# Kernel optimization log

Measured on AMD Instinct MI355X. Metric: run time of the kernel, lower is better.

The kernel has to match this reference:

```python
import jax, jax.numpy as jnp
import numpy as np

B, T, I, H, O = 64, 512, 256, 1024, 512
STEPS = 100


def _lstm_cell(x, h, c, Wih, Whh, b):
    # torch gate order: i, f, g, o ; Wih:[4H,in], Whh:[4H,H]
    g = x @ Wih.T + h @ Whh.T + b
    i, f, gg, o = jnp.split(g, 4, axis=-1)
    c = jax.nn.sigmoid(f) * c + jax.nn.sigmoid(i) * jnp.tanh(gg)
    h = jax.nn.sigmoid(o) * jnp.tanh(c)
    return h, c


def setup_inputs() -> dict:
    key = jax.random.key(0)
    ks = jax.random.split(key, 11)
    s = 1.0 / np.sqrt(H)  # torch nn.LSTM init scale
    f32 = jnp.float32
    return {
        "inputs": jax.random.normal(ks[0], (B, T, I), f32),
        "enc_Wih": jax.random.normal(ks[1], (4 * H, I), f32) * s,
        "enc_Whh": jax.random.normal(ks[2], (4 * H, H), f32) * s,
        "enc_bih": jax.random.normal(ks[3], (4 * H,), f32) * s,
        "enc_bhh": jax.random.normal(ks[4], (4 * H,), f32) * s,
        "dec_Wih": jax.random.normal(ks[5], (4 * H, O), f32) * s,
        "dec_Whh": jax.random.normal(ks[6], (4 * H, H), f32) * s,
        "dec_bih": jax.random.normal(ks[7], (4 * H,), f32) * s,
        "dec_bhh": jax.random.normal(ks[8], (4 * H,), f32) * s,
        "fc_W": jax.random.normal(ks[9], (O, H), f32) * s,
        "fc_b": jax.random.normal(ks[10], (O,), f32) * s,
    }


def reference(inputs, enc_Wih, enc_Whh, enc_bih, enc_bhh,
              dec_Wih, dec_Whh, dec_bih, dec_bhh, fc_W, fc_b):
    b_enc = enc_bih + enc_bhh
    b_dec = dec_bih + dec_bhh
    Bz = inputs.shape[0]
    h0 = jnp.zeros((Bz, H), inputs.dtype)
    c0 = jnp.zeros((Bz, H), inputs.dtype)

    # ---- encoder LSTM over time (batch_first input -> scan over T) ----
    def enc_step(carry, x_t):
        h, c = carry
        h, c = _lstm_cell(x_t, h, c, enc_Wih, enc_Whh, b_enc)
        return (h, c), None

    (h, c), _ = jax.lax.scan(enc_step, (h0, c0), inputs.transpose(1, 0, 2))

    def dec_step(carry, _):
        inp, h, c = carry
        h, c = _lstm_cell(inp, h, c, dec_Wih, dec_Whh, b_dec)
        logits = h @ fc_W.T + fc_b                 # [B, O]
        tok = jnp.argmax(logits, axis=-1)          # [B]
        # next decoder input: predicted token index broadcast to feature dim
        nxt = jnp.broadcast_to(tok[:, None].astype(inputs.dtype), (Bz, O))
        return (nxt, h, c), tok

    init_inp = jnp.zeros((Bz, O), inputs.dtype)
    _, toks = jax.lax.scan(dec_step, (init_inp, h, c), None, length=STEPS)
    # toks: [STEPS, B] -> [B, STEPS, 1] to match torch cat of (B,1,1) tokens
    return toks.T[:, :, None].astype(jnp.int64)
```

## Files before the change

### kernel.cpp

```cpp
#include <hip/hip_runtime.h>
#include <cstdint>
#include <cmath>

#define BB 64
#define TT 512
#define NI 256
#define HH 1024
#define NO 512
#define NSTEPS 100
#define KT 64
#define NBLK 256
#define NTHR 512
#define NCTR 64

__device__ unsigned g_arr[(NCTR + 1) * 32];
__device__ float g_hA[HH * BB];
__device__ float g_hB[HH * BB];
__device__ float g_cst[HH * BB];
__device__ float g_dsum[4 * HH];
__device__ float g_logits[NO * BB];
__device__ float g_xt[TT * NI * BB];

__device__ __forceinline__ float sigf(float x) { return 1.0f / (1.0f + expf(-x)); }

__device__ __forceinline__ float2 ldh2(const float* p) {
  unsigned long long u = __hip_atomic_load((const unsigned long long*)p,
                                           __ATOMIC_RELAXED, __HIP_MEMORY_SCOPE_AGENT);
  union { unsigned long long u; float2 f; } c; c.u = u; return c.f;
}
__device__ __forceinline__ float ldc1(const float* p) {
  unsigned u = __hip_atomic_load((const unsigned*)p,
                                 __ATOMIC_RELAXED, __HIP_MEMORY_SCOPE_AGENT);
  union { unsigned u; float f; } c; c.u = u; return c.f;
}
__device__ __forceinline__ void stc1(float* p, float v) {
  union { float f; unsigned u; } c; c.f = v;
  __hip_atomic_store((unsigned*)p, c.u, __ATOMIC_RELAXED, __HIP_MEMORY_SCOPE_AGENT);
}

__device__ __forceinline__ void bar_arrive(int blk) {
  __syncthreads();
  if (threadIdx.x == 0) {
    __hip_atomic_fetch_add(&g_arr[(blk & (NCTR - 1)) * 32], 1u,
                           __ATOMIC_RELAXED, __HIP_MEMORY_SCOPE_AGENT);
  }
}

__device__ __forceinline__ void bar_wait(int blk, unsigned n) {
  if (threadIdx.x == 0) {
    if (blk == 0) {
      for (;;) {
        unsigned tot = 0;
        #pragma unroll
        for (int i = 0; i < NCTR; ++i)
          tot += __hip_atomic_load(&g_arr[i * 32], __ATOMIC_RELAXED, __HIP_MEMORY_SCOPE_AGENT);
        if (tot >= n * NBLK) break;
        __builtin_amdgcn_s_sleep(1);
      }
      __hip_atomic_store(&g_arr[NCTR * 32], n, __ATOMIC_RELAXED, __HIP_MEMORY_SCOPE_AGENT);
    } else {
      while (__hip_atomic_load(&g_arr[NCTR * 32], __ATOMIC_RELAXED, __HIP_MEMORY_SCOPE_AGENT) < n)
        __builtin_amdgcn_s_sleep(2);
    }
  }
  __syncthreads();
}

__global__ void reset_counter() {
  if (threadIdx.x <= NCTR) g_arr[threadIdx.x * 32] = 0u;
}

#define LOAD_A_X(asrc) \
  { ah0 = *(const float2*)&(asrc)[tid * 2]; \
    ah1 = *(const float2*)&(asrc)[tid * 2 + 1024]; \
    ah2 = *(const float2*)&(asrc)[tid * 2 + 2048]; \
    ah3 = *(const float2*)&(asrc)[tid * 2 + 3072]; }
#define LOAD_A_H(asrc) \
  { ah0 = ldh2(&(asrc)[tid * 2]); \
    ah1 = ldh2(&(asrc)[tid * 2 + 1024]); \
    ah2 = ldh2(&(asrc)[tid * 2 + 2048]); \
    ah3 = ldh2(&(asrc)[tid * 2 + 3072]); }
#define LOAD_W2(wsrc, ld, k) \
  { const float* wp = (wsrc) + (size_t)grow0 * (ld) + (k) + kkl; \
    wr0 = wp[0]; wr1 = wp[(size_t)(ld)]; }

#define STORE_LDS(bufi) \
  { float* ab = &As[bufi][0][0]; \
    *(float2*)&ab[tid * 2]        = ah0; \
    *(float2*)&ab[tid * 2 + 1024] = ah1; \
    *(float2*)&ab[tid * 2 + 2048] = ah2; \
    *(float2*)&ab[tid * 2 + 3072] = ah3; \
    float2 w2; w2.x = wr0; w2.y = wr1; \
    *(float2*)&Wt[bufi][kkl][r0] = w2; }

#define FMA_CHUNK(bufi) \
  _Pragma("unroll") \
  for (int kk2 = 0; kk2 < 2; ++kk2) { \
    const int kk = kt2 * 2 + kk2; \
    float4 a0 = *(const float4*)&As[bufi][kk][cg * 8]; \
    float4 a1 = *(const float4*)&As[bufi][kk][cg * 8 + 4]; \
    float4 w0 = *(const float4*)&Wt[bufi][kk][rg * 8]; \
    float4 w1 = *(const float4*)&Wt[bufi][kk][rg * 8 + 4]; \
    float av[8] = {a0.x, a0.y, a0.z, a0.w, a1.x, a1.y, a1.z, a1.w}; \
    float wv[8] = {w0.x, w0.y, w0.z, w0.w, w1.x, w1.y, w1.z, w1.w}; \
    _Pragma("unroll") for (int r = 0; r < 8; ++r) \
      _Pragma("unroll") for (int c = 0; c < 8; ++c) \
        acc[r][c] = fmaf(wv[r], av[c], acc[r][c]); \
  }

__global__ void __launch_bounds__(NTHR, 1)
seq2seq_kernel(const float* __restrict__ xin,
               const float* __restrict__ eWih, const float* __restrict__ eWhh,
               const float* __restrict__ ebih, const float* __restrict__ ebhh,
               const float* __restrict__ dWih, const float* __restrict__ dWhh,
               const float* __restrict__ dbih, const float* __restrict__ dbhh,
               const float* __restrict__ fcW,  const float* __restrict__ fcb,
               int* __restrict__ out)
{
  __shared__ __align__(16) float As[2][KT][BB];
  __shared__ __align__(16) float Wt[2][KT][20];
  __shared__ __align__(16) float Gp[16][17][68];
  __shared__ float avals[8][BB];
  __shared__ int   aidx[8][BB];
  __shared__ float ptok[BB];

  const int tid = threadIdx.x;
  const int blk = blockIdx.x;
  unsigned sync_no = 0;

  const int wv  = tid >> 6;
  const int ln  = tid & 63;
  const int hi  = ln >> 5;
  const int l5  = ln & 31;
  const int ks16 = (wv << 1) | (l5 >> 4);
  const int kt2  = ks16 * 2 + hi;
  const int rg  = (l5 >> 3) & 1;
  const int cg  = l5 & 7;
  const int jj2 = (tid >> 6) & 3;
  const int cb  = tid & 63;
  const int j2  = blk * 4 + jj2;
  const int r0  = wv * 2;
  const int kkl = ln;
  const int grow0 = ((r0 >> 2) * HH + blk * 4 + (r0 & 3));
  const int ktd = tid >> 4;
  const int cgd = tid & 15;
  float* const Gpd = &Gp[0][0][0];

  {
    if (tid < 256) {
      int idx = blk * 256 + tid;
      stc1(&g_hA[idx], 0.0f);
      g_cst[idx] = 0.0f;
    }
    int r = blk * 16 + (tid >> 5);
    int l32 = tid & 31;
    const float* wrp = dWih + (size_t)r * NO;
    float s = 0.0f;
    for (int k = l32; k < NO; k += 32) s += wrp[k];
    for (int off = 16; off; off >>= 1) s += __shfl_down(s, off, 32);
    if (l32 == 0) stc1(&g_dsum[r], s);
    for (int w = blk * NTHR + tid; w < TT * NI * BB; w += NBLK * NTHR) {
      int b = w & 63;
      int tk = w >> 6;
      int k = tk & (NI - 1);
      int t = tk >> 8;
      stc1(&g_xt[w], xin[((size_t)b * TT + t) * NI + k]);
    }
  }
  const float be0 = ebih[j2]          + ebhh[j2];
  const float be1 = ebih[HH + j2]     + ebhh[HH + j2];
  const float be2 = ebih[2 * HH + j2] + ebhh[2 * HH + j2];
  const float be3 = ebih[3 * HH + j2] + ebhh[3 * HH + j2];
  bar_arrive(blk); ++sync_no; bar_wait(blk, sync_no);

  const float* hc = g_hA;
  float* hn = g_hB;

  float2 ah0, ah1, ah2, ah3;
  float wr0, wr1;
  LOAD_A_X(g_xt);
  LOAD_W2(eWih, NI, 0);

  for (int t = 0; t < TT; ++t) {
    float acc[8][8];
    #pragma unroll
    for (int r = 0; r < 8; ++r)
      #pragma unroll
      for (int c = 0; c < 8; ++c) acc[r][c] = 0.0f;

    STORE_LDS(0);
    for (int ch = 0; ch < 20; ++ch) {
      const int buf = ch & 1;
      if (ch == 3) bar_wait(blk, sync_no);
      if (ch + 1 < 20) {
        const int c1 = ch + 1;
        if (c1 < 4) {
          LOAD_A_X(g_xt + ((size_t)t * NI + c1 * KT) * BB);
          LOAD_W2(eWih, NI, c1 * KT);
        } else {
          LOAD_A_H(hc + (size_t)(c1 * KT - NI) * BB);
          LOAD_W2(eWhh, HH, c1 * KT - NI);
        }
      }
      __syncthreads();
      FMA_CHUNK(buf);
      if (ch + 1 < 20) STORE_LDS(buf ^ 1);
    }
    #pragma unroll
    for (int r = 0; r < 8; ++r)
      #pragma unroll
      for (int c = 0; c < 8; ++c)
        acc[r][c] += __shfl_xor(acc[r][c], 32);
    __syncthreads();
    if (hi == 0) {
      #pragma unroll
      for (int r = 0; r < 8; ++r) {
        float4 v0 = {acc[r][0], acc[r][1], acc[r][2], acc[r][3]};
        float4 v1 = {acc[r][4], acc[r][5], acc[r][6], acc[r][7]};
        *(float4*)&Gp[ks16][rg * 8 + r][cg * 8]     = v0;
        *(float4*)&Gp[ks16][rg * 8 + r][cg * 8 + 4] = v1;
      }
    }
    __syncthreads();
    if (tid < 256) {
      float gsum[4];
      #pragma unroll
      for (int g = 0; g < 4; ++g) {
        const int rt = g * 4 + jj2;
        float s = 0.0f;
        #pragma unroll
        for (int q = 0; q < 16; ++q) s += Gp[q][rt][cb];
        gsum[g] = s;
      }
      float pi = gsum[0] + be0;
      float pf = gsum[1] + be1;
      float pg = gsum[2] + be2;
      float po = gsum[3] + be3;
      float co = g_cst[(size_t)j2 * BB + cb];
      float cn = sigf(pf) * co + sigf(pi) * tanhf(pg);
      float hv = sigf(po) * tanhf(cn);
      g_cst[(size_t)j2 * BB + cb] = cn;
      stc1(&hn[(size_t)j2 * BB + cb], hv);
    }
    {
      const int tn = (t + 1 < TT) ? t + 1 : t;
      LOAD_A_X(g_xt + (size_t)tn * NI * BB);
      LOAD_W2(eWih, NI, 0);
    }
    bar_arrive(blk); ++sync_no;
    float* tmp = (float*)hc; hc = hn; hn = tmp;
  }
  if (tid < BB) ptok[tid] = 0.0f;
  bar_wait(blk, sync_no);

  const float bd0 = dbih[j2]          + dbhh[j2];
  const float bd1 = dbih[HH + j2]     + dbhh[HH + j2];
  const float bd2 = dbih[2 * HH + j2] + dbhh[2 * HH + j2];
  const float bd3 = dbih[3 * HH + j2] + dbhh[3 * HH + j2];
  const float ds0 = g_dsum[j2];
  const float ds1 = g_dsum[HH + j2];
  const float ds2 = g_dsum[2 * HH + j2];
  const float ds3 = g_dsum[3 * HH + j2];
  LOAD_A_H(hc);
  LOAD_W2(dWhh, HH, 0);

  for (int s = 0; s < NSTEPS; ++s) {
    float acc[8][8];
    #pragma unroll
    for (int r = 0; r < 8; ++r)
      #pragma unroll
      for (int c = 0; c < 8; ++c) acc[r][c] = 0.0f;

    STORE_LDS(0);
    for (int ch = 0; ch < 16; ++ch) {
      const int buf = ch & 1;
      if (ch + 1 < 16) {
        LOAD_A_H(hc + (size_t)(ch + 1) * KT * BB);
        LOAD_W2(dWhh, HH, (ch + 1) * KT);
      }
      __syncthreads();
      FMA_CHUNK(buf);
      if (ch + 1 < 16) STORE_LDS(buf ^ 1);
    }
    #pragma unroll
    for (int r = 0; r < 8; ++r)
      #pragma unroll
      for (int c = 0; c < 8; ++c)
        acc[r][c] += __shfl_xor(acc[r][c], 32);
    __syncthreads();
    if (hi == 0) {
      #pragma unroll
      for (int r = 0; r < 8; ++r) {
        float4 v0 = {acc[r][0], acc[r][1], acc[r][2], acc[r][3]};
        float4 v1 = {acc[r][4], acc[r][5], acc[r][6], acc[r][7]};
        *(float4*)&Gp[ks16][rg * 8 + r][cg * 8]     = v0;
        *(float4*)&Gp[ks16][rg * 8 + r][cg * 8 + 4] = v1;
      }
    }
    __syncthreads();
    if (tid < 256) {
      float gsum[4];
      #pragma unroll
      for (int g = 0; g < 4; ++g) {
        const int rt = g * 4 + jj2;
        float ssum = 0.0f;
        #pragma unroll
        for (int q = 0; q < 16; ++q) ssum += Gp[q][rt][cb];
        gsum[g] = ssum;
      }
      float tk = ptok[cb];
      float pi = gsum[0] + bd0 + tk * ds0;
      float pf = gsum[1] + bd1 + tk * ds1;
      float pg = gsum[2] + bd2 + tk * ds2;
      float po = gsum[3] + bd3 + tk * ds3;
      float co = g_cst[(size_t)j2 * BB + cb];
      float cn = sigf(pf) * co + sigf(pi) * tanhf(pg);
      float hv = sigf(po) * tanhf(cn);
      g_cst[(size_t)j2 * BB + cb] = cn;
      stc1(&hn[(size_t)j2 * BB + cb], hv);
    }
    float fw0 = 0.0f;
    if (blk < 128) fw0 = fcW[(size_t)(blk * 4 + ((tid >> 6) & 3)) * HH + kkl];
    bar_arrive(blk); ++sync_no; bar_wait(blk, sync_no);
    { float* tmp = (float*)hc; hc = hn; hn = tmp; }

    if (blk < 128) {
      float facc[4][4];
      #pragma unroll
      for (int r = 0; r < 4; ++r)
        #pragma unroll
        for (int c = 0; c < 4; ++c) facc[r][c] = 0.0f;

      float fw = fw0;
      LOAD_A_H(hc);
      { float* ab = &As[0][0][0];
        *(float2*)&ab[tid * 2]        = ah0;
        *(float2*)&ab[tid * 2 + 1024] = ah1;
        *(float2*)&ab[tid * 2 + 2048] = ah2;
        *(float2*)&ab[tid * 2 + 3072] = ah3;
        Wt[0][kkl][(tid >> 6) & 3] = fw; }
      for (int ch = 0; ch < 16; ++ch) {
        const int buf = ch & 1;
        if (ch + 1 < 16) {
          LOAD_A_H(hc + (size_t)(ch + 1) * KT * BB);
          fw = fcW[(size_t)(blk * 4 + ((tid >> 6) & 3)) * HH + (ch + 1) * KT + kkl];
        }
        __syncthreads();
        #pragma unroll
        for (int kk2 = 0; kk2 < 2; ++kk2) {
          const int kk = ktd * 2 + kk2;
          float4 a = *(const float4*)&As[buf][kk][cgd * 4];
          float4 w = *(const float4*)&Wt[buf][kk][0];
          float av[4] = {a.x, a.y, a.z, a.w};
          float wvv[4] = {w.x, w.y, w.z, w.w};
          #pragma unroll
          for (int r = 0; r < 4; ++r)
            #pragma unroll
            for (int c = 0; c < 4; ++c)
              facc[r][c] = fmaf(wvv[r], av[c], facc[r][c]);
        }
        if (ch + 1 < 16) {
          float* ab = &As[buf ^ 1][0][0];
          *(float2*)&ab[tid * 2]        = ah0;
          *(float2*)&ab[tid * 2 + 1024] = ah1;
          *(float2*)&ab[tid * 2 + 2048] = ah2;
          *(float2*)&ab[tid * 2 + 3072] = ah3;
          Wt[buf ^ 1][kkl][(tid >> 6) & 3] = fw;
        }
      }
      __syncthreads();
      #pragma unroll
      for (int r = 0; r < 4; ++r) {
        float4 v = {facc[r][0], facc[r][1], facc[r][2], facc[r][3]};
        *(float4*)&Gpd[ktd * 272 + r * 68 + cgd * 4] = v;
      }
      __syncthreads();
      if (tid < 256) {
        const int oo = tid >> 6, ob = tid & 63;
        float ssum = 0.0f;
        #pragma unroll
        for (int q = 0; q < 32; ++q) ssum += Gpd[q * 272 + oo * 68 + ob];
        const int o = blk * 4 + oo;
        stc1(&g_logits[(size_t)o * BB + ob], ssum + fcb[o]);
      }
    }
    LOAD_A_H(hc);
    LOAD_W2(dWhh, HH, 0);
    bar_arrive(blk); ++sync_no; bar_wait(blk, sync_no);

    {
      const int q = tid >> 6, b = tid & 63;
      float bv = -3.402823466e38f; int bo = 0;
      #pragma unroll
      for (int g = 0; g < 4; ++g) {
        float lv[16];
        #pragma unroll
        for (int i = 0; i < 16; ++i)
          lv[i] = ldc1(&g_logits[(size_t)(q * 64 + g * 16 + i) * BB + b]);
        #pragma unroll
        for (int i = 0; i < 16; ++i)
          if (lv[i] > bv) { bv = lv[i]; bo = q * 64 + g * 16 + i; }
      }
      avals[q][b] = bv; aidx[q][b] = bo;
    }
    __syncthreads();
    if (tid < BB) {
      float bv = avals[0][tid]; int bo = aidx[0][tid];
      #pragma unroll
      for (int q = 1; q < 8; ++q)
        if (avals[q][tid] > bv) { bv = avals[q][tid]; bo = aidx[q][tid]; }
      ptok[tid] = (float)bo;
      if (blk == 0) out[(size_t)tid * NSTEPS + s] = bo;
    }
    __syncthreads();
  }
}

extern "C" void kernel_launch(void* const* d_in, const int* in_sizes, int n_in,
                              void* d_out, int out_size, void* d_ws, size_t ws_size,
                              hipStream_t stream) {
  (void)in_sizes; (void)n_in; (void)out_size; (void)d_ws; (void)ws_size;
  const float* xin  = (const float*)d_in[0];
  const float* eWih = (const float*)d_in[1];
  const float* eWhh = (const float*)d_in[2];
  const float* ebih = (const float*)d_in[3];
  const float* ebhh = (const float*)d_in[4];
  const float* dWih = (const float*)d_in[5];
  const float* dWhh = (const float*)d_in[6];
  const float* dbih = (const float*)d_in[7];
  const float* dbhh = (const float*)d_in[8];
  const float* fcW  = (const float*)d_in[9];
  const float* fcb  = (const float*)d_in[10];
  int* out = (int*)d_out;

  reset_counter<<<1, 128, 0, stream>>>();
  seq2seq_kernel<<<NBLK, NTHR, 0, stream>>>(
      xin, eWih, eWhh, ebih, ebhh, dWih, dWhh, dbih, dbhh, fcW, fcb, out);
}
```

Measured before the change: 15.38 ms.

## Keep per-block LSTM weights resident in LDS and streamline grid barrier

Each persistent block now preloads its 16 gate rows of the encoder weights (and later the decoder Whh and fc rows) into a swizzled LDS buffer once, instead of re-reading the weight slices from global memory on every timestep. The activation tile loads become plain float4 loads into an XOR-swizzled LDS layout, replacing per-element atomic loads, and an acquire fence after the barrier keeps them correct. The K split changes so partial sums are reduced with two shuffles and half as many LDS partials. The grid barrier's counter sum is spread across a wavefront with shuffle reduction. This uses much more LDS and depends on the fence for cross-block visibility of h and logits.

```diff
diff --git a/kernel.cpp b/kernel.cpp
--- a/kernel.cpp
+++ b/kernel.cpp
@@ -14,25 +14,15 @@
 #define NCTR 64
 
 __device__ unsigned g_arr[(NCTR + 1) * 32];
-__device__ float g_hA[HH * BB];
-__device__ float g_hB[HH * BB];
-__device__ float g_cst[HH * BB];
-__device__ float g_dsum[4 * HH];
-__device__ float g_logits[NO * BB];
-__device__ float g_xt[TT * NI * BB];
+__device__ __align__(16) float g_hA[HH * BB];
+__device__ __align__(16) float g_hB[HH * BB];
+__device__ __align__(16) float g_cst[HH * BB];
+__device__ __align__(16) float g_dsum[4 * HH];
+__device__ __align__(16) float g_logits[NO * BB];
+__device__ __align__(16) float g_xt[TT * NI * BB];
 
 __device__ __forceinline__ float sigf(float x) { return 1.0f / (1.0f + expf(-x)); }
 
-__device__ __forceinline__ float2 ldh2(const float* p) {
-  unsigned long long u = __hip_atomic_load((const unsigned long long*)p,
-                                           __ATOMIC_RELAXED, __HIP_MEMORY_SCOPE_AGENT);
-  union { unsigned long long u; float2 f; } c; c.u = u; return c.f;
-}
-__device__ __forceinline__ float ldc1(const float* p) {
-  unsigned u = __hip_atomic_load((const unsigned*)p,
-                                 __ATOMIC_RELAXED, __HIP_MEMORY_SCOPE_AGENT);
-  union { unsigned u; float f; } c; c.u = u; return c.f;
-}
 __device__ __forceinline__ void stc1(float* p, float v) {
   union { float f; unsigned u; } c; c.f = v;
   __hip_atomic_store((unsigned*)p, c.u, __ATOMIC_RELAXED, __HIP_MEMORY_SCOPE_AGENT);
@@ -47,65 +37,57 @@
 }
 
 __device__ __forceinline__ void bar_wait(int blk, unsigned n) {
-  if (threadIdx.x == 0) {
-    if (blk == 0) {
+  if (blk == 0) {
+    if (threadIdx.x < 64) {
       for (;;) {
-        unsigned tot = 0;
-        #pragma unroll
-        for (int i = 0; i < NCTR; ++i)
-          tot += __hip_atomic_load(&g_arr[i * 32], __ATOMIC_RELAXED, __HIP_MEMORY_SCOPE_AGENT);
-        if (tot >= n * NBLK) break;
+        unsigned v = __hip_atomic_load(&g_arr[threadIdx.x * 32],
+                                       __ATOMIC_RELAXED, __HIP_MEMORY_SCOPE_AGENT);
+        #pragma unroll
+        for (int off = 32; off; off >>= 1) v += __shfl_xor(v, off);
+        if (v >= n * NBLK) break;
         __builtin_amdgcn_s_sleep(1);
       }
-      __hip_atomic_store(&g_arr[NCTR * 32], n, __ATOMIC_RELAXED, __HIP_MEMORY_SCOPE_AGENT);
-    } else {
-      while (__hip_atomic_load(&g_arr[NCTR * 32], __ATOMIC_RELAXED, __HIP_MEMORY_SCOPE_AGENT) < n)
-        __builtin_amdgcn_s_sleep(2);
-    }
+      if (threadIdx.x == 0)
+        __hip_atomic_store(&g_arr[NCTR * 32], n, __ATOMIC_RELAXED,
+                           __HIP_MEMORY_SCOPE_AGENT);
+    }
+  } else if (threadIdx.x == 0) {
+    while (__hip_atomic_load(&g_arr[NCTR * 32], __ATOMIC_RELAXED,
+                             __HIP_MEMORY_SCOPE_AGENT) < n)
+      __builtin_amdgcn_s_sleep(1);
   }
   __syncthreads();
+  __builtin_amdgcn_fence(__ATOMIC_ACQUIRE, "agent");
 }
 
 __global__ void reset_counter() {
   if (threadIdx.x <= NCTR) g_arr[threadIdx.x * 32] = 0u;
 }
 
-#define LOAD_A_X(asrc) \
-  { ah0 = *(const float2*)&(asrc)[tid * 2]; \
-    ah1 = *(const float2*)&(asrc)[tid * 2 + 1024]; \
-    ah2 = *(const float2*)&(asrc)[tid * 2 + 2048]; \
-    ah3 = *(const float2*)&(asrc)[tid * 2 + 3072]; }
-#define LOAD_A_H(asrc) \
-  { ah0 = ldh2(&(asrc)[tid * 2]); \
-    ah1 = ldh2(&(asrc)[tid * 2 + 1024]); \
-    ah2 = ldh2(&(asrc)[tid * 2 + 2048]); \
-    ah3 = ldh2(&(asrc)[tid * 2 + 3072]); }
-#define LOAD_W2(wsrc, ld, k) \
-  { const float* wp = (wsrc) + (size_t)grow0 * (ld) + (k) + kkl; \
-    wr0 = wp[0]; wr1 = wp[(size_t)(ld)]; }
-
-#define STORE_LDS(bufi) \
-  { float* ab = &As[bufi][0][0]; \
-    *(float2*)&ab[tid * 2]        = ah0; \
-    *(float2*)&ab[tid * 2 + 1024] = ah1; \
-    *(float2*)&ab[tid * 2 + 2048] = ah2; \
-    *(float2*)&ab[tid * 2 + 3072] = ah3; \
-    float2 w2; w2.x = wr0; w2.y = wr1; \
-    *(float2*)&Wt[bufi][kkl][r0] = w2; }
-
-#define FMA_CHUNK(bufi) \
+#define LOAD_A(asrc) \
+  { ah0 = *(const float4*)&(asrc)[tid * 4]; \
+    ah1 = *(const float4*)&(asrc)[tid * 4 + 2048]; }
+
+#define STORE_A(bufi) \
+  { float* ab = &AsF[(bufi) * 4096]; \
+    *(float4*)&ab[a_st] = ah0; \
+    *(float4*)&ab[a_st + 2048] = ah1; }
+
+#define FMA_CHUNK(bufi, wch) \
   _Pragma("unroll") \
   for (int kk2 = 0; kk2 < 2; ++kk2) { \
     const int kk = kt2 * 2 + kk2; \
-    float4 a0 = *(const float4*)&As[bufi][kk][cg * 8]; \
-    float4 a1 = *(const float4*)&As[bufi][kk][cg * 8 + 4]; \
-    float4 w0 = *(const float4*)&Wt[bufi][kk][rg * 8]; \
-    float4 w1 = *(const float4*)&Wt[bufi][kk][rg * 8 + 4]; \
-    float av[8] = {a0.x, a0.y, a0.z, a0.w, a1.x, a1.y, a1.z, a1.w}; \
-    float wv[8] = {w0.x, w0.y, w0.z, w0.w, w1.x, w1.y, w1.z, w1.w}; \
+    const float* abp = &AsF[(bufi) * 4096 + (kk << 6)]; \
+    const float* wbp = &Wall[((wch) << 10) + (kk << 4)]; \
+    float4 a0 = *(const float4*)(abp + slA0); \
+    float4 a1 = *(const float4*)(abp + slA1); \
+    float4 w0 = *(const float4*)(wbp + slW0); \
+    float4 w1 = *(const float4*)(wbp + slW1); \
+    float av8[8] = {a0.x, a0.y, a0.z, a0.w, a1.x, a1.y, a1.z, a1.w}; \
+    float wv8[8] = {w0.x, w0.y, w0.z, w0.w, w1.x, w1.y, w1.z, w1.w}; \
     _Pragma("unroll") for (int r = 0; r < 8; ++r) \
       _Pragma("unroll") for (int c = 0; c < 8; ++c) \
-        acc[r][c] = fmaf(wv[r], av[c], acc[r][c]); \
+        acc[r][c] = fmaf(wv8[r], av8[c], acc[r][c]); \
   }
 
 __global__ void __launch_bounds__(NTHR, 1)
@@ -117,9 +99,9 @@
                const float* __restrict__ fcW,  const float* __restrict__ fcb,
                int* __restrict__ out)
 {
-  __shared__ __align__(16) float As[2][KT][BB];
-  __shared__ __align__(16) float Wt[2][KT][20];
-  __shared__ __align__(16) float Gp[16][17][68];
+  __shared__ __align__(16) float AsF[2 * 4096];
+  __shared__ __align__(16) float Wall[20 * KT * 16];
+  __shared__ __align__(16) float Gp[8][17][68];
   __shared__ float avals[8][BB];
   __shared__ int   aidx[8][BB];
   __shared__ float ptok[BB];
@@ -132,18 +114,21 @@
   const int ln  = tid & 63;
   const int hi  = ln >> 5;
   const int l5  = ln & 31;
-  const int ks16 = (wv << 1) | (l5 >> 4);
-  const int kt2  = ks16 * 2 + hi;
+  const int kt2 = (((wv << 1) | (l5 >> 4)) << 1) | hi;
   const int rg  = (l5 >> 3) & 1;
   const int cg  = l5 & 7;
   const int jj2 = (tid >> 6) & 3;
   const int cb  = tid & 63;
   const int j2  = blk * 4 + jj2;
-  const int r0  = wv * 2;
-  const int kkl = ln;
-  const int grow0 = ((r0 >> 2) * HH + blk * 4 + (r0 & 3));
   const int ktd = tid >> 4;
   const int cgd = tid & 15;
+  const int sq   = kt2 & 3;
+  const int slA0 = ((cg * 2)     ^ sq) << 2;
+  const int slA1 = ((cg * 2 + 1) ^ sq) << 2;
+  const int slW0 = ((rg * 2)     ^ sq) << 2;
+  const int slW1 = ((rg * 2 + 1) ^ sq) << 2;
+  const int slD  = (cgd ^ (ktd & 3)) << 2;
+  const int a_st = ((tid >> 4) << 6) | (((tid & 15) ^ ((tid >> 5) & 3)) << 2);
   float* const Gpd = &Gp[0][0][0];
 
   {
@@ -152,13 +137,13 @@
       stc1(&g_hA[idx], 0.0f);
       g_cst[idx] = 0.0f;
     }
-    int r = blk * 16 + (tid >> 5);
+    int rr = blk * 16 + (tid >> 5);
     int l32 = tid & 31;
-    const float* wrp = dWih + (size_t)r * NO;
+    const float* wrp = dWih + (size_t)rr * NO;
     float s = 0.0f;
     for (int k = l32; k < NO; k += 32) s += wrp[k];
     for (int off = 16; off; off >>= 1) s += __shfl_down(s, off, 32);
-    if (l32 == 0) stc1(&g_dsum[r], s);
+    if (l32 == 0) stc1(&g_dsum[rr], s);
     for (int w = blk * NTHR + tid; w < TT * NI * BB; w += NBLK * NTHR) {
       int b = w & 63;
       int tk = w >> 6;
@@ -166,6 +151,17 @@
       int t = tk >> 8;
       stc1(&g_xt[w], xin[((size_t)b * TT + t) * NI + k]);
     }
+    for (int r2 = 0; r2 < 16; ++r2) {
+      const int growr = (r2 >> 2) * HH + blk * 4 + (r2 & 3);
+      for (int c0 = 0; c0 < NI + HH; c0 += NTHR) {
+        const int c = c0 + tid;
+        if (c < NI + HH) {
+          const float w = (c < NI) ? eWih[(size_t)growr * NI + c]
+                                   : eWhh[(size_t)growr * HH + (c - NI)];
+          Wall[c * 16 + ((((r2 >> 2) ^ ((c >> 1) & 3)) << 2) | (r2 & 3))] = w;
+        }
+      }
+    }
   }
   const float be0 = ebih[j2]          + ebhh[j2];
   const float be1 = ebih[HH + j2]     + ebhh[HH + j2];
@@ -176,10 +172,8 @@
   const float* hc = g_hA;
   float* hn = g_hB;
 
-  float2 ah0, ah1, ah2, ah3;
-  float wr0, wr1;
-  LOAD_A_X(g_xt);
-  LOAD_W2(eWih, NI, 0);
+  float4 ah0, ah1;
+  LOAD_A(g_xt);
 
   for (int t = 0; t < TT; ++t) {
     float acc[8][8];
@@ -188,37 +182,37 @@
       #pragma unroll
       for (int c = 0; c < 8; ++c) acc[r][c] = 0.0f;
 
-    STORE_LDS(0);
+    STORE_A(0);
+    #pragma unroll 2
     for (int ch = 0; ch < 20; ++ch) {
       const int buf = ch & 1;
       if (ch == 3) bar_wait(blk, sync_no);
       if (ch + 1 < 20) {
         const int c1 = ch + 1;
-        if (c1 < 4) {
-          LOAD_A_X(g_xt + ((size_t)t * NI + c1 * KT) * BB);
-          LOAD_W2(eWih, NI, c1 * KT);
-        } else {
-          LOAD_A_H(hc + (size_t)(c1 * KT - NI) * BB);
-          LOAD_W2(eWhh, HH, c1 * KT - NI);
-        }
+        const float* asrc = (c1 < 4)
+            ? g_xt + ((size_t)t * NI + c1 * KT) * BB
+            : hc + (size_t)(c1 * KT - NI) * BB;
+        LOAD_A(asrc);
       }
       __syncthreads();
-      FMA_CHUNK(buf);
-      if (ch + 1 < 20) STORE_LDS(buf ^ 1);
+      FMA_CHUNK(buf, ch);
+      if (ch + 1 < 20) STORE_A(buf ^ 1);
     }
     #pragma unroll
     for (int r = 0; r < 8; ++r)
       #pragma unroll
-      for (int c = 0; c < 8; ++c)
+      for (int c = 0; c < 8; ++c) {
         acc[r][c] += __shfl_xor(acc[r][c], 32);
-    __syncthreads();
-    if (hi == 0) {
+        acc[r][c] += __shfl_xor(acc[r][c], 16);
+      }
+    __syncthreads();
+    if (ln < 16) {
       #pragma unroll
       for (int r = 0; r < 8; ++r) {
         float4 v0 = {acc[r][0], acc[r][1], acc[r][2], acc[r][3]};
         float4 v1 = {acc[r][4], acc[r][5], acc[r][6], acc[r][7]};
-        *(float4*)&Gp[ks16][rg * 8 + r][cg * 8]     = v0;
-        *(float4*)&Gp[ks16][rg * 8 + r][cg * 8 + 4] = v1;
+        *(float4*)&Gp[wv][rg * 8 + r][cg * 8]     = v0;
+        *(float4*)&Gp[wv][rg * 8 + r][cg * 8 + 4] = v1;
       }
     }
     __syncthreads();
@@ -227,10 +221,10 @@
       #pragma unroll
       for (int g = 0; g < 4; ++g) {
         const int rt = g * 4 + jj2;
-        float s = 0.0f;
-        #pragma unroll
-        for (int q = 0; q < 16; ++q) s += Gp[q][rt][cb];
-        gsum[g] = s;
+        float ssum = 0.0f;
+        #pragma unroll
+        for (int q = 0; q < 8; ++q) ssum += Gp[q][rt][cb];
+        gsum[g] = ssum;
       }
       float pi = gsum[0] + be0;
       float pf = gsum[1] + be1;
@@ -244,14 +238,30 @@
     }
     {
       const int tn = (t + 1 < TT) ? t + 1 : t;
-      LOAD_A_X(g_xt + (size_t)tn * NI * BB);
-      LOAD_W2(eWih, NI, 0);
+      LOAD_A(g_xt + (size_t)tn * NI * BB);
     }
     bar_arrive(blk); ++sync_no;
-    float* tmp = (float*)hc; hc = hn; hn = tmp;
+    { float* tmp = (float*)hc; hc = hn; hn = tmp; }
   }
   if (tid < BB) ptok[tid] = 0.0f;
   bar_wait(blk, sync_no);
+
+  for (int r2 = 0; r2 < 16; ++r2) {
+    const int growr = (r2 >> 2) * HH + blk * 4 + (r2 & 3);
+    for (int c0 = 0; c0 < HH; c0 += NTHR) {
+      const int c = c0 + tid;
+      const float w = dWhh[(size_t)growr * HH + c];
+      Wall[c * 16 + ((((r2 >> 2) ^ ((c >> 1) & 3)) << 2) | (r2 & 3))] = w;
+    }
+  }
+  if (blk < 128) {
+    for (int e = tid; e < 4096; e += NTHR) {
+      const int rr = e >> 10;
+      const int c = e & 1023;
+      Wall[16384 + c * 4 + rr] = fcW[(size_t)(blk * 4 + rr) * HH + c];
+    }
+  }
+  __syncthreads();
 
   const float bd0 = dbih[j2]          + dbhh[j2];
   const float bd1 = dbih[HH + j2]     + dbhh[HH + j2];
@@ -261,8 +271,7 @@
   const float ds1 = g_dsum[HH + j2];
   const float ds2 = g_dsum[2 * HH + j2];
   const float ds3 = g_dsum[3 * HH + j2];
-  LOAD_A_H(hc);
-  LOAD_W2(dWhh, HH, 0);
+  LOAD_A(hc);
 
   for (int s = 0; s < NSTEPS; ++s) {
     float acc[8][8];
@@ -271,30 +280,30 @@
       #pragma unroll
       for (int c = 0; c < 8; ++c) acc[r][c] = 0.0f;
 
-    STORE_LDS(0);
+    STORE_A(0);
+    #pragma unroll 2
     for (int ch = 0; ch < 16; ++ch) {
       const int buf = ch & 1;
-      if (ch + 1 < 16) {
-        LOAD_A_H(hc + (size_t)(ch + 1) * KT * BB);
-        LOAD_W2(dWhh, HH, (ch + 1) * KT);
-      }
+      if (ch + 1 < 16) LOAD_A(hc + (size_t)(ch + 1) * KT * BB);
       __syncthreads();
-      FMA_CHUNK(buf);
-      if (ch + 1 < 16) STORE_LDS(buf ^ 1);
+      FMA_CHUNK(buf, ch);
+      if (ch + 1 < 16) STORE_A(buf ^ 1);
     }
     #pragma unroll
     for (int r = 0; r < 8; ++r)
       #pragma unroll
-      for (int c = 0; c < 8; ++c)
+      for (int c = 0; c < 8; ++c) {
         acc[r][c] += __shfl_xor(acc[r][c], 32);
-    __syncthreads();
-    if (hi == 0) {
+        acc[r][c] += __shfl_xor(acc[r][c], 16);
+      }
+    __syncthreads();
+    if (ln < 16) {
       #pragma unroll
       for (int r = 0; r < 8; ++r) {
         float4 v0 = {acc[r][0], acc[r][1], acc[r][2], acc[r][3]};
         float4 v1 = {acc[r][4], acc[r][5], acc[r][6], acc[r][7]};
-        *(float4*)&Gp[ks16][rg * 8 + r][cg * 8]     = v0;
-        *(float4*)&Gp[ks16][rg * 8 + r][cg * 8 + 4] = v1;
+        *(float4*)&Gp[wv][rg * 8 + r][cg * 8]     = v0;
+        *(float4*)&Gp[wv][rg * 8 + r][cg * 8 + 4] = v1;
       }
     }
     __syncthreads();
@@ -305,7 +314,7 @@
         const int rt = g * 4 + jj2;
         float ssum = 0.0f;
         #pragma unroll
-        for (int q = 0; q < 16; ++q) ssum += Gp[q][rt][cb];
+        for (int q = 0; q < 8; ++q) ssum += Gp[q][rt][cb];
         gsum[g] = ssum;
       }
       float tk = ptok[cb];
@@ -319,8 +328,6 @@
       g_cst[(size_t)j2 * BB + cb] = cn;
       stc1(&hn[(size_t)j2 * BB + cb], hv);
     }
-    float fw0 = 0.0f;
-    if (blk < 128) fw0 = fcW[(size_t)(blk * 4 + ((tid >> 6) & 3)) * HH + kkl];
     bar_arrive(blk); ++sync_no; bar_wait(blk, sync_no);
     { float* tmp = (float*)hc; hc = hn; hn = tmp; }
 
@@ -331,42 +338,27 @@
         #pragma unroll
         for (int c = 0; c < 4; ++c) facc[r][c] = 0.0f;
 
-      float fw = fw0;
-      LOAD_A_H(hc);
-      { float* ab = &As[0][0][0];
-        *(float2*)&ab[tid * 2]        = ah0;
-        *(float2*)&ab[tid * 2 + 1024] = ah1;
-        *(float2*)&ab[tid * 2 + 2048] = ah2;
-        *(float2*)&ab[tid * 2 + 3072] = ah3;
-        Wt[0][kkl][(tid >> 6) & 3] = fw; }
+      LOAD_A(hc);
+      STORE_A(0);
+      #pragma unroll 2
       for (int ch = 0; ch < 16; ++ch) {
         const int buf = ch & 1;
-        if (ch + 1 < 16) {
-          LOAD_A_H(hc + (size_t)(ch + 1) * KT * BB);
-          fw = fcW[(size_t)(blk * 4 + ((tid >> 6) & 3)) * HH + (ch + 1) * KT + kkl];
-        }
+        if (ch + 1 < 16) LOAD_A(hc + (size_t)(ch + 1) * KT * BB);
         __syncthreads();
         #pragma unroll
         for (int kk2 = 0; kk2 < 2; ++kk2) {
           const int kk = ktd * 2 + kk2;
-          float4 a = *(const float4*)&As[buf][kk][cgd * 4];
-          float4 w = *(const float4*)&Wt[buf][kk][0];
-          float av[4] = {a.x, a.y, a.z, a.w};
-          float wvv[4] = {w.x, w.y, w.z, w.w};
+          float4 a = *(const float4*)&AsF[buf * 4096 + (kk << 6) + slD];
+          float4 w = *(const float4*)&Wall[16384 + (((ch << 6) + kk) << 2)];
+          float av4[4] = {a.x, a.y, a.z, a.w};
+          float wv4[4] = {w.x, w.y, w.z, w.w};
           #pragma unroll
           for (int r = 0; r < 4; ++r)
             #pragma unroll
             for (int c = 0; c < 4; ++c)
-              facc[r][c] = fmaf(wvv[r], av[c], facc[r][c]);
+              facc[r][c] = fmaf(wv4[r], av4[c], facc[r][c]);
         }
-        if (ch + 1 < 16) {
-          float* ab = &As[buf ^ 1][0][0];
-          *(float2*)&ab[tid * 2]        = ah0;
-          *(float2*)&ab[tid * 2 + 1024] = ah1;
-          *(float2*)&ab[tid * 2 + 2048] = ah2;
-          *(float2*)&ab[tid * 2 + 3072] = ah3;
-          Wt[buf ^ 1][kkl][(tid >> 6) & 3] = fw;
-        }
+        if (ch + 1 < 16) STORE_A(buf ^ 1);
       }
       __syncthreads();
       #pragma unroll
@@ -384,8 +376,7 @@
         stc1(&g_logits[(size_t)o * BB + ob], ssum + fcb[o]);
       }
     }
-    LOAD_A_H(hc);
-    LOAD_W2(dWhh, HH, 0);
+    LOAD_A(hc);
     bar_arrive(blk); ++sync_no; bar_wait(blk, sync_no);
 
     {
@@ -396,7 +387,7 @@
         float lv[16];
         #pragma unroll
         for (int i = 0; i < 16; ++i)
-          lv[i] = ldc1(&g_logits[(size_t)(q * 64 + g * 16 + i) * BB + b]);
+          lv[i] = g_logits[(size_t)(q * 64 + g * 16 + i) * BB + b];
         #pragma unroll
         for (int i = 0; i < 16; ++i)
           if (lv[i] > bv) { bv = lv[i]; bo = q * 64 + g * 16 + i; }
```

Measured after the change: 22.00 ms. +43.1%, slower.
